# Performance work log

Hardware: AMD Instinct MI355X
Metric: run time of the kernel (lower is better)

The kernel has to match this reference:

```python
import jax, jax.numpy as jnp
import numpy as np

B, H, W, DIM, HEADS, WS = 32, 56, 56, 192, 6, 7
KD = DIM // HEADS          # key_dim = head_dim = 32 (attn_ratio=1.0 -> d = KD, dh = DIM)
DH = KD * HEADS
HQKV = DH + 2 * KD * HEADS # 576
L = H * W
HIDDEN = 4 * DIM
NWIN = (H // WS) * (W // WS)
NTOK = WS * WS
SCALE = KD ** -0.5


def _bias_idxs(ws):
    pts = [(i, j) for i in range(ws) for j in range(ws)]
    offs, idxs = {}, []
    for p1 in pts:
        for p2 in pts:
            o = (abs(p1[0] - p2[0]), abs(p1[1] - p2[1]))
            if o not in offs:
                offs[o] = len(offs)
            idxs.append(offs[o])
    return np.asarray(idxs, np.int32).reshape(ws * ws, ws * ws), len(offs)

BIAS_IDX, NOFF = _bias_idxs(WS)  # [49,49], 49 distinct offsets


def _ln(x, g, b, eps=1e-5):
    m = x.mean(-1, keepdims=True)
    v = jnp.mean((x - m) ** 2, -1, keepdims=True)
    return (x - m) * jax.lax.rsqrt(v + eps) * g + b


def setup_inputs() -> dict:
    key = jax.random.key(0)
    ks = jax.random.split(key, 8)
    f32 = jnp.float32
    return {
        "x": jax.random.normal(ks[0], (B, L, DIM), f32),
        "ln1_g": jnp.ones((DIM,), f32), "ln1_b": jnp.zeros((DIM,), f32),
        "qkv_w": jax.random.normal(ks[1], (DIM, HQKV), f32) * 0.02,
        "qkv_b": jnp.zeros((HQKV,), f32),
        "proj_w": jax.random.normal(ks[2], (DH, DIM), f32) * 0.02,
        "proj_b": jnp.zeros((DIM,), f32),
        "attn_bias": jax.random.normal(ks[3], (HEADS, NOFF), f32) * 0.02,
        "conv_w": jax.random.normal(ks[4], (DIM, 1, 3, 3), f32) * 0.1,  # depthwise OIHW
        "bn_g": jnp.ones((DIM,), f32), "bn_b": jnp.zeros((DIM,), f32),
        "bn_m": jnp.zeros((DIM,), f32), "bn_v": jnp.ones((DIM,), f32),
        "ln2_g": jnp.ones((DIM,), f32), "ln2_b": jnp.zeros((DIM,), f32),
        "fc1_w": jax.random.normal(ks[5], (DIM, HIDDEN), f32) * 0.02,
        "fc1_b": jnp.zeros((HIDDEN,), f32),
        "fc2_w": jax.random.normal(ks[6], (HIDDEN, DIM), f32) * 0.02,
        "fc2_b": jnp.zeros((DIM,), f32),
    }


def reference(x, ln1_g, ln1_b, qkv_w, qkv_b, proj_w, proj_b, attn_bias,
              conv_w, bn_g, bn_b, bn_m, bn_v, ln2_g, ln2_b,
              fc1_w, fc1_b, fc2_w, fc2_b):
    # ---- window partition: [B,L,C] -> [B*nWin, 49, C] (H,W divisible by WS, no pad)
    xw = x.reshape(B, H // WS, WS, W // WS, WS, DIM)
    xw = xw.transpose(0, 1, 3, 2, 4, 5).reshape(B * NWIN, NTOK, DIM)
    # ---- attention (pre-LN inside Attention module)
    h = _ln(xw, ln1_g, ln1_b)
    qkv = (h @ qkv_w + qkv_b).reshape(B * NWIN, NTOK, HEADS, 3 * KD)
    qkv = qkv.transpose(0, 2, 1, 3)                      # [Bw, heads, N, 3*KD]
    q, k, v = qkv[..., :KD], qkv[..., KD:2 * KD], qkv[..., 2 * KD:]
    bias = attn_bias[:, BIAS_IDX]                        # [heads, 49, 49] gathered table
    scores = jnp.einsum('bhnd,bhmd->bhnm', q, k) * SCALE + bias[None]
    a = jax.nn.softmax(scores, axis=-1)
    o = jnp.einsum('bhnm,bhmd->bhnd', a, v)
    o = o.transpose(0, 2, 1, 3).reshape(B * NWIN, NTOK, DH)
    o = o @ proj_w + proj_b
    # ---- window unpartition -> [B,L,C], residual add
    o = o.reshape(B, H // WS, W // WS, WS, WS, DIM)
    o = o.transpose(0, 1, 3, 2, 4, 5).reshape(B, L, DIM)
    x = x + o
    # ---- depthwise 3x3 conv + BN (eval-mode) in NCHW
    xc = x.transpose(0, 2, 1).reshape(B, DIM, H, W)
    xc = jax.lax.conv_general_dilated(
        xc, conv_w, window_strides=(1, 1), padding=[(1, 1), (1, 1)],
        feature_group_count=DIM, dimension_numbers=('NCHW', 'OIHW', 'NCHW'))
    inv = jax.lax.rsqrt(bn_v + 1e-5)
    xc = (xc - bn_m[None, :, None, None]) * (inv * bn_g)[None, :, None, None] + bn_b[None, :, None, None]
    x = xc.reshape(B, DIM, L).transpose(0, 2, 1)
    # ---- MLP (LN -> fc1 -> GELU(exact) -> fc2) with residual
    h2 = _ln(x, ln2_g, ln2_b)
    h2 = jax.nn.gelu(h2 @ fc1_w + fc1_b, approximate=False)
    h2 = h2 @ fc2_w + fc2_b
    return x + h2
```

## Files before the change

kernel.cpp:

```cpp
#include <hip/hip_runtime.h>
#include <hip/hip_bf16.h>

#define DIMC 192
#define LTOT 3136

using bf16x8 = __attribute__((ext_vector_type(8))) short;
using f32x4  = __attribute__((ext_vector_type(4))) float;

static __device__ __forceinline__ unsigned short f2bf(float f) {
  unsigned u = __builtin_bit_cast(unsigned, f);
  u = (u + 0x7FFFu + ((u >> 16) & 1u)) >> 16;
  return (unsigned short)u;
}
static __device__ __forceinline__ float bf2f(unsigned short u) {
  unsigned v = ((unsigned)u) << 16;
  return __builtin_bit_cast(float, v);
}
static __device__ __forceinline__ int iabs(int a) { return a < 0 ? -a : a; }

static __device__ __forceinline__ void gload16(const unsigned short* g, unsigned short* lds) {
  __builtin_amdgcn_global_load_lds(
      (const __attribute__((address_space(1))) void*)g,
      (__attribute__((address_space(3))) void*)lds, 16, 0, 0);
}

__global__ __launch_bounds__(256) void prep_k(
    const float* __restrict__ qkv_w, const float* __restrict__ proj_w,
    const float* __restrict__ fc1_w, const float* __restrict__ fc2_w,
    const float* __restrict__ conv_w,
    const float* __restrict__ bn_g, const float* __restrict__ bn_b,
    const float* __restrict__ bn_m, const float* __restrict__ bn_v,
    unsigned short* __restrict__ qkvT, unsigned short* __restrict__ projT,
    unsigned short* __restrict__ fc1T, unsigned short* __restrict__ fc2T,
    float* __restrict__ convT, float* __restrict__ bnsc, float* __restrict__ bnsh)
{
  int idx = blockIdx.x * 256 + threadIdx.x;
  if (idx < 122880) { int n = idx / 192, k = idx % 192;
    qkvT[idx] = (n < 576) ? f2bf(qkv_w[k * 576 + n]) : 0; return; }
  idx -= 122880;
  if (idx < 49152)  { int n = idx / 192, k = idx % 192;
    projT[idx] = (n < 192) ? f2bf(proj_w[k * 192 + n]) : 0; return; }
  idx -= 49152;
  if (idx < 147456) { int n = idx / 192, k = idx % 192;
    fc1T[idx] = f2bf(fc1_w[k * 768 + n]); return; }
  idx -= 147456;
  if (idx < 196608) { int n = idx / 768, k = idx % 768;
    fc2T[idx] = (n < 192) ? f2bf(fc2_w[k * 192 + n]) : 0; return; }
  idx -= 196608;
  if (idx < 1728)   { int tap = idx / 192, c = idx % 192; convT[idx] = conv_w[c * 9 + tap]; return; }
  idx -= 1728;
  if (idx < 192) {
    float s = bn_g[idx] * rsqrtf(bn_v[idx] + 1e-5f);
    bnsc[idx] = s; bnsh[idx] = bn_b[idx] - bn_m[idx] * s;
  }
}

__global__ __launch_bounds__(256) void ln1_k(
    const float* __restrict__ x, const float* __restrict__ g,
    const float* __restrict__ b, unsigned short* __restrict__ h1)
{
  const int grp = threadIdx.x >> 6, l = threadIdx.x & 63;
  const int m = blockIdx.x * 4 + grp;
  const int w = m / 49, t = m % 49;
  const int bb = w >> 6, win = w & 63;
  const int lpix = ((win >> 3) * 7 + t / 7) * 56 + (win & 7) * 7 + t % 7;
  const float* row = x + ((size_t)bb * LTOT + lpix) * DIMC;
  const bool act = l < 48;
  const int c = l * 4;
  float4 v = make_float4(0.f, 0.f, 0.f, 0.f);
  if (act) v = *(const float4*)(row + c);
  float s = v.x + v.y + v.z + v.w;
  float ss = v.x * v.x + v.y * v.y + v.z * v.z + v.w * v.w;
  #pragma unroll
  for (int off = 1; off < 64; off <<= 1) { s += __shfl_xor(s, off); ss += __shfl_xor(ss, off); }
  float mean = s * (1.f / 192.f);
  float rstd = rsqrtf(ss * (1.f / 192.f) - mean * mean + 1e-5f);
  if (act) {
    float4 gg = *(const float4*)(g + c);
    float4 bv = *(const float4*)(b + c);
    ushort4 o;
    o.x = f2bf((v.x - mean) * rstd * gg.x + bv.x);
    o.y = f2bf((v.y - mean) * rstd * gg.y + bv.y);
    o.z = f2bf((v.z - mean) * rstd * gg.z + bv.z);
    o.w = f2bf((v.w - mean) * rstd * gg.w + bv.w);
    *(ushort4*)(h1 + (size_t)m * DIMC + c) = o;
  }
}

__global__ __launch_bounds__(256) void qkvg_k(
    const unsigned short* __restrict__ h1, const unsigned short* __restrict__ qkvT,
    const float* __restrict__ qkv_b, unsigned short* __restrict__ qkv)
{
  __shared__ unsigned short Wc[12288];
  const int tid = threadIdx.x;
  const int l = tid & 63, wv = tid >> 6;
  const int u = l >> 4, ll = l & 15;
  const int m0 = blockIdx.x * 64;

  bf16x8 areg[6];
  {
    const unsigned short* arow = h1 + (size_t)(m0 + wv * 16 + ll) * 192;
    #pragma unroll
    for (int kk = 0; kk < 6; ++kk)
      areg[kk] = *(const bf16x8*)(arow + kk * 32 + u * 8);
  }
  for (int c = 0; c < 9; ++c) {
    if (c) __syncthreads();
    const char* Wg = (const char*)(qkvT + (size_t)c * 64 * 192);
    #pragma unroll
    for (int i = 0; i < 6; ++i) {
      int ob = i * 4096 + tid * 16;
      int r = ob / 384, cc = ob % 384;
      int cs = cc ^ ((r & 7) << 4);
      gload16((const unsigned short*)(Wg + r * 384 + cs), &Wc[ob >> 1]);
    }
    __syncthreads();
    f32x4 p1[4] = {};
    #pragma unroll
    for (int kk = 0; kk < 6; ++kk) {
      int cb = (kk * 64 + u * 16) ^ ((ll & 7) << 4);
      #pragma unroll
      for (int nf = 0; nf < 4; ++nf) {
        bf16x8 bfr = *(const bf16x8*)((const char*)Wc + (nf * 16 + ll) * 384 + cb);
        p1[nf] = __builtin_amdgcn_mfma_f32_16x16x32_bf16(areg[kk], bfr, p1[nf], 0, 0, 0);
      }
    }
    #pragma unroll
    for (int nf = 0; nf < 4; ++nf)
    #pragma unroll
    for (int r = 0; r < 4; ++r) {
      int m = m0 + wv * 16 + u * 4 + r;
      int n = c * 64 + nf * 16 + ll;
      qkv[(size_t)m * 576 + n] = f2bf(p1[nf][r] + qkv_b[n]);
    }
  }
}

__global__ __launch_bounds__(256) void attnp_k(
    const unsigned short* __restrict__ qkv, const float* __restrict__ attn_bias,
    const unsigned short* __restrict__ projT, const float* __restrict__ proj_b,
    const float* __restrict__ x, unsigned short* __restrict__ x1b)
{
  __shared__ unsigned short Qs[2560];
  __shared__ unsigned short Ks[2560];
  __shared__ unsigned short Vt[2304];
  __shared__ unsigned short Ps[4608];
  __shared__ float bias_s[52];
  const int tid = threadIdx.x;
  const int l = tid & 63, wv = tid >> 6;
  const int u = l >> 4, ll = l & 15;
  const int w = blockIdx.x, b = w >> 6, win = w & 63;
  const f32x4 fz = {0.f, 0.f, 0.f, 0.f};

  for (int i = tid; i < 15 * 40; i += 256) {
    Qs[(49 + i / 40) * 40 + i % 40] = 0;
    Ks[(49 + i / 40) * 40 + i % 40] = 0;
  }
  for (int i = tid; i < 32 * 15; i += 256) Vt[(i / 15) * 72 + 49 + i % 15] = 0;

  f32x4 pacc[4][3] = {};

  for (int h = 0; h < 6; ++h) {
    __syncthreads();
    if (tid < 49) bias_s[tid] = attn_bias[h * 49 + tid];
    #pragma unroll
    for (int it = 0; it < 3; ++it) {
      int idx = tid + it * 256;
      if (idx < 588) {
        int row = idx / 12, g = idx % 12;
        int4 v = *(const int4*)&qkv[((size_t)w * 49 + row) * 576 + h * 96 + g * 8];
        if (g < 4) *(int4*)&Qs[row * 40 + g * 8] = v;
        else if (g < 8) *(int4*)&Ks[row * 40 + (g - 4) * 8] = v;
        else {
          union { int4 v4; unsigned short us[8]; } uu; uu.v4 = v;
          int d0 = (g - 8) * 8;
          #pragma unroll
          for (int e = 0; e < 8; ++e) Vt[(d0 + e) * 72 + row] = uu.us[e];
        }
      }
    }
    __syncthreads();

    {
      const int qr = wv * 16 + ll;
      const int qi = qr > 48 ? 48 : qr;
      bf16x8 qf = *(const bf16x8*)&Qs[(wv * 16 + ll) * 40 + u * 8];
      f32x4 sc[4];
      #pragma unroll
      for (int kt = 0; kt < 4; ++kt) {
        bf16x8 kf = *(const bf16x8*)&Ks[(kt * 16 + ll) * 40 + u * 8];
        sc[kt] = __builtin_amdgcn_mfma_f32_16x16x32_bf16(kf, qf, fz, 0, 0, 0);
      }
      float sv[4][4];
      float mx = -1e30f;
      #pragma unroll
      for (int kt = 0; kt < 4; ++kt)
        #pragma unroll
        for (int r = 0; r < 4; ++r) {
          int kr = kt * 16 + u * 4 + r;
          float val = -1e30f;
          if (kr < 49)
            val = sc[kt][r] * 0.17677669529663689f +
                  bias_s[iabs(qi / 7 - kr / 7) * 7 + iabs(qi % 7 - kr % 7)];
          sv[kt][r] = val;
          mx = fmaxf(mx, val);
        }
      mx = fmaxf(mx, __shfl_xor(mx, 16));
      mx = fmaxf(mx, __shfl_xor(mx, 32));
      float sum = 0.f;
      #pragma unroll
      for (int kt = 0; kt < 4; ++kt)
        #pragma unroll
        for (int r = 0; r < 4; ++r) {
          float p = __expf(sv[kt][r] - mx);
          sv[kt][r] = p; sum += p;
        }
      sum += __shfl_xor(sum, 16);
      sum += __shfl_xor(sum, 32);
      float inv = 1.f / sum;
      #pragma unroll
      for (int kt = 0; kt < 4; ++kt)
        #pragma unroll
        for (int r = 0; r < 4; ++r)
          Ps[(wv * 16 + ll) * 72 + kt * 16 + u * 4 + r] = f2bf(sv[kt][r] * inv);
    }
    __syncthreads();

    {
      f32x4 oa[2] = {fz, fz};
      #pragma unroll
      for (int kk = 0; kk < 2; ++kk) {
        bf16x8 pf = *(const bf16x8*)&Ps[(wv * 16 + ll) * 72 + kk * 32 + u * 8];
        #pragma unroll
        for (int nt = 0; nt < 2; ++nt) {
          bf16x8 vf = *(const bf16x8*)&Vt[(nt * 16 + ll) * 72 + kk * 32 + u * 8];
          oa[nt] = __builtin_amdgcn_mfma_f32_16x16x32_bf16(pf, vf, oa[nt], 0, 0, 0);
        }
      }
      #pragma unroll
      for (int nt = 0; nt < 2; ++nt)
        #pragma unroll
        for (int r = 0; r < 4; ++r)
          Qs[(wv * 16 + u * 4 + r) * 40 + nt * 16 + ll] = f2bf(oa[nt][r]);
    }
    __syncthreads();

    {
      bf16x8 af[4], bfr[3];
      #pragma unroll
      for (int mt = 0; mt < 4; ++mt)
        af[mt] = *(const bf16x8*)&Qs[(mt * 16 + ll) * 40 + u * 8];
      #pragma unroll
      for (int nf = 0; nf < 3; ++nf)
        bfr[nf] = *(const bf16x8*)&projT[(size_t)(wv * 48 + nf * 16 + ll) * 192 + h * 32 + u * 8];
      #pragma unroll
      for (int mt = 0; mt < 4; ++mt)
        #pragma unroll
        for (int nf = 0; nf < 3; ++nf)
          pacc[mt][nf] = __builtin_amdgcn_mfma_f32_16x16x32_bf16(af[mt], bfr[nf], pacc[mt][nf], 0, 0, 0);
    }
  }

  #pragma unroll
  for (int mt = 0; mt < 4; ++mt)
  #pragma unroll
  for (int r = 0; r < 4; ++r) {
    int m = mt * 16 + u * 4 + r;
    if (m < 49) {
      int lpix = ((win >> 3) * 7 + m / 7) * 56 + (win & 7) * 7 + m % 7;
      size_t base = ((size_t)b * LTOT + lpix) * DIMC;
      #pragma unroll
      for (int nf = 0; nf < 3; ++nf) {
        int n = wv * 48 + nf * 16 + ll;
        float val = pacc[mt][nf][r] + proj_b[n] + x[base + n];
        x1b[base + n] = f2bf(val);
      }
    }
  }
}

__global__ __launch_bounds__(256) void fmlp_k(
    const unsigned short* __restrict__ h2, const unsigned short* __restrict__ fc1T,
    const float* __restrict__ fc1_b, const unsigned short* __restrict__ fc2T,
    const float* __restrict__ fc2_b, const unsigned short* __restrict__ x2,
    float* __restrict__ out)
{
  __shared__ unsigned short W1[6144];
  __shared__ unsigned short W2[6144];
  __shared__ unsigned short P[2048];
  const int tid = threadIdx.x;
  const int l = tid & 63, wv = tid >> 6;
  const int u = l >> 4, ll = l & 15;
  const int m0 = blockIdx.x * 64;
  f32x4 acc[12] = {};

  bf16x8 areg[6];
  {
    const unsigned short* arow = h2 + (size_t)(m0 + wv * 16 + ll) * 192;
    #pragma unroll
    for (int kk = 0; kk < 6; ++kk)
      areg[kk] = *(const bf16x8*)(arow + kk * 32 + u * 8);
  }

  for (int c = 0; c < 24; ++c) {
    if (c) __syncthreads();
    const char* W1g = (const char*)(fc1T + (size_t)c * 32 * 192);
    #pragma unroll
    for (int i = 0; i < 3; ++i) {
      int ob = i * 4096 + tid * 16;
      int r = ob / 384, cc = ob % 384;
      int cs = cc ^ ((r & 7) << 4);
      gload16((const unsigned short*)(W1g + r * 384 + cs), &W1[ob >> 1]);
    }
    #pragma unroll
    for (int i = 0; i < 3; ++i) {
      int unit = i * 256 + tid;
      int r = unit >> 2, q = unit & 3;
      int4 vv = *(const int4*)&fc2T[(size_t)r * 768 + c * 32 + q * 8];
      *(int4*)((char*)W2 + r * 64 + ((q * 16) ^ ((r & 3) << 4))) = vv;
    }
    __syncthreads();

    {
      f32x4 p1[2] = {};
      #pragma unroll
      for (int kk = 0; kk < 6; ++kk) {
        int cb = (kk * 64 + u * 16) ^ ((ll & 7) << 4);
        #pragma unroll
        for (int nf = 0; nf < 2; ++nf) {
          bf16x8 bfr = *(const bf16x8*)((const char*)W1 + (nf * 16 + ll) * 384 + cb);
          p1[nf] = __builtin_amdgcn_mfma_f32_16x16x32_bf16(areg[kk], bfr, p1[nf], 0, 0, 0);
        }
      }
      #pragma unroll
      for (int nf = 0; nf < 2; ++nf)
      #pragma unroll
      for (int r = 0; r < 4; ++r) {
        int mrow = wv * 16 + u * 4 + r;
        int n = nf * 16 + ll;
        float v = p1[nf][r] + fc1_b[c * 32 + n];
        float gl = v / (1.f + __expf(-1.5957691216057308f * (v + 0.044715f * v * v * v)));
        *(unsigned short*)((char*)P + mrow * 64 + ((n * 2) ^ ((mrow & 3) << 4))) = f2bf(gl);
      }
    }
    {
      bf16x8 af2 = *(const bf16x8*)((const char*)P + (wv * 16 + ll) * 64 +
                                    ((u * 16) ^ ((ll & 3) << 4)));
      #pragma unroll
      for (int nt = 0; nt < 12; ++nt) {
        bf16x8 bfr = *(const bf16x8*)((const char*)W2 + (nt * 16 + ll) * 64 +
                                      ((u * 16) ^ ((ll & 3) << 4)));
        acc[nt] = __builtin_amdgcn_mfma_f32_16x16x32_bf16(af2, bfr, acc[nt], 0, 0, 0);
      }
    }
  }
  #pragma unroll
  for (int nt = 0; nt < 12; ++nt)
  #pragma unroll
  for (int r = 0; r < 4; ++r) {
    int m = m0 + wv * 16 + u * 4 + r;
    int n = nt * 16 + ll;
    size_t o = (size_t)m * 192 + n;
    out[o] = acc[nt][r] + fc2_b[n] + bf2f(x2[o]);
  }
}

__global__ __launch_bounds__(256) void conv_k(
    const unsigned short* __restrict__ x1b, const float* __restrict__ wT,
    const float* __restrict__ bnsc, const float* __restrict__ bnsh,
    const float* __restrict__ g2, const float* __restrict__ b2,
    unsigned short* __restrict__ x2, unsigned short* __restrict__ h2)
{
  const int bid = blockIdx.x;
  const int swz = (bid & 7) * 3136 + (bid >> 3);
  const int grp = threadIdx.x >> 6, l = threadIdx.x & 63;
  const int gid = swz * 4 + grp;
  const int b = gid / LTOT, p = gid % LTOT;
  const int i = p / 56, j = p % 56;
  const bool act = l < 48;
  const int c = l * 4;
  float4 acc = make_float4(0.f, 0.f, 0.f, 0.f);
  if (act) {
    #pragma unroll
    for (int di = -1; di <= 1; ++di) {
      int ni = i + di;
      if (ni < 0 || ni >= 56) continue;
      #pragma unroll
      for (int dj = -1; dj <= 1; ++dj) {
        int nj = j + dj;
        if (nj < 0 || nj >= 56) continue;
        ushort4 sv = *(const ushort4*)&x1b[((size_t)b * LTOT + ni * 56 + nj) * DIMC + c];
        float4 wv = *(const float4*)&wT[((di + 1) * 3 + (dj + 1)) * DIMC + c];
        acc.x += bf2f(sv.x) * wv.x; acc.y += bf2f(sv.y) * wv.y;
        acc.z += bf2f(sv.z) * wv.z; acc.w += bf2f(sv.w) * wv.w;
      }
    }
    float4 s4 = *(const float4*)&bnsc[c];
    float4 h4 = *(const float4*)&bnsh[c];
    acc.x = acc.x * s4.x + h4.x; acc.y = acc.y * s4.y + h4.y;
    acc.z = acc.z * s4.z + h4.z; acc.w = acc.w * s4.w + h4.w;
    ushort4 xv;
    xv.x = f2bf(acc.x); xv.y = f2bf(acc.y); xv.z = f2bf(acc.z); xv.w = f2bf(acc.w);
    *(ushort4*)&x2[(size_t)gid * DIMC + c] = xv;
  }
  float s = act ? acc.x + acc.y + acc.z + acc.w : 0.f;
  float ss = act ? acc.x * acc.x + acc.y * acc.y + acc.z * acc.z + acc.w * acc.w : 0.f;
  #pragma unroll
  for (int off = 1; off < 64; off <<= 1) { s += __shfl_xor(s, off); ss += __shfl_xor(ss, off); }
  float mean = s * (1.f / 192.f);
  float rstd = rsqrtf(ss * (1.f / 192.f) - mean * mean + 1e-5f);
  if (act) {
    float4 gg = *(const float4*)&g2[c];
    float4 bb = *(const float4*)&b2[c];
    ushort4 ov;
    ov.x = f2bf((acc.x - mean) * rstd * gg.x + bb.x);
    ov.y = f2bf((acc.y - mean) * rstd * gg.y + bb.y);
    ov.z = f2bf((acc.z - mean) * rstd * gg.z + bb.z);
    ov.w = f2bf((acc.w - mean) * rstd * gg.w + bb.w);
    *(ushort4*)&h2[(size_t)gid * DIMC + c] = ov;
  }
}

extern "C" void kernel_launch(void* const* d_in, const int* in_sizes, int n_in,
                              void* d_out, int out_size, void* d_ws, size_t ws_size,
                              hipStream_t stream) {
  const float* x      = (const float*)d_in[0];
  const float* ln1_g  = (const float*)d_in[1];
  const float* ln1_b  = (const float*)d_in[2];
  const float* qkv_w  = (const float*)d_in[3];
  const float* qkv_b  = (const float*)d_in[4];
  const float* proj_w = (const float*)d_in[5];
  const float* proj_b = (const float*)d_in[6];
  const float* attn_b = (const float*)d_in[7];
  const float* conv_w = (const float*)d_in[8];
  const float* bn_g   = (const float*)d_in[9];
  const float* bn_b   = (const float*)d_in[10];
  const float* bn_m   = (const float*)d_in[11];
  const float* bn_v   = (const float*)d_in[12];
  const float* ln2_g  = (const float*)d_in[13];
  const float* ln2_b  = (const float*)d_in[14];
  const float* fc1_w  = (const float*)d_in[15];
  const float* fc1_b  = (const float*)d_in[16];
  const float* fc2_w  = (const float*)d_in[17];
  const float* fc2_b  = (const float*)d_in[18];
  float* out = (float*)d_out;

  const size_t AOFF = 1048576, BOFF = AOFF + 115605504;
  const size_t NEEDED = BOFF + 38535168;
  if (ws_size < NEEDED) return;

  char* ws = (char*)d_ws;
  unsigned short* qkvT  = (unsigned short*)(ws);
  unsigned short* projT = (unsigned short*)(ws + 245760);
  unsigned short* fc1T  = (unsigned short*)(ws + 344064);
  unsigned short* fc2T  = (unsigned short*)(ws + 638976);
  float*          convT = (float*)(ws + 1032192);
  float*          bnsc  = (float*)(ws + 1039104);
  float*          bnsh  = (float*)(ws + 1039872);

  unsigned short* qkv = (unsigned short*)(ws + AOFF);
  unsigned short* x2  = (unsigned short*)(ws + AOFF);
  unsigned short* h2  = (unsigned short*)(ws + AOFF + 38535168);
  unsigned short* h1  = (unsigned short*)(ws + BOFF);
  unsigned short* x1b = (unsigned short*)(ws + BOFF);

  prep_k<<<2024, 256, 0, stream>>>(qkv_w, proj_w, fc1_w, fc2_w, conv_w,
                                   bn_g, bn_b, bn_m, bn_v,
                                   qkvT, projT, fc1T, fc2T, convT, bnsc, bnsh);
  ln1_k<<<25088, 256, 0, stream>>>(x, ln1_g, ln1_b, h1);
  qkvg_k<<<1568, 256, 0, stream>>>(h1, qkvT, qkv_b, qkv);
  attnp_k<<<2048, 256, 0, stream>>>(qkv, attn_b, projT, proj_b, x, x1b);
  conv_k<<<25088, 256, 0, stream>>>(x1b, convT, bnsc, bnsh, ln2_g, ln2_b, x2, h2);
  fmlp_k<<<1568, 256, 0, stream>>>(h2, fc1T, fc1_b, fc2T, fc2_b, x2, out);
}
```

Measured before the change: 379.9 us.

## Double-buffer fc1/fc2 weight tiles in fused MLP kernel to overlap loads

The fused MLP kernel now keeps two LDS buffers each for the fc1 and fc2 weight chunks. While chunk c is being computed, it issues the global-to-LDS loads for fc1 chunk c+1 and register loads for fc2 chunk c+1, writing the fc2 data to LDS after compute. This cuts the per-iteration barrier from two to one and hides load latency behind MFMA work. The cost is roughly double the LDS footprint, which may reduce blocks per CU, plus extra register pressure from holding the prefetched fc2 data.

```diff
diff --git a/kernel.cpp b/kernel.cpp
--- a/kernel.cpp
+++ b/kernel.cpp
@@ -285,8 +285,8 @@
     const float* __restrict__ fc2_b, const unsigned short* __restrict__ x2,
     float* __restrict__ out)
 {
-  __shared__ unsigned short W1[6144];
-  __shared__ unsigned short W2[6144];
+  __shared__ unsigned short W1[2][6144];
+  __shared__ unsigned short W2[2][6144];
   __shared__ unsigned short P[2048];
   const int tid = threadIdx.x;
   const int l = tid & 63, wv = tid >> 6;
@@ -302,24 +302,47 @@
       areg[kk] = *(const bf16x8*)(arow + kk * 32 + u * 8);
   }
 
-  for (int c = 0; c < 24; ++c) {
-    if (c) __syncthreads();
-    const char* W1g = (const char*)(fc1T + (size_t)c * 32 * 192);
+  {
+    const char* W1g = (const char*)(fc1T);
     #pragma unroll
     for (int i = 0; i < 3; ++i) {
       int ob = i * 4096 + tid * 16;
       int r = ob / 384, cc = ob % 384;
       int cs = cc ^ ((r & 7) << 4);
-      gload16((const unsigned short*)(W1g + r * 384 + cs), &W1[ob >> 1]);
+      gload16((const unsigned short*)(W1g + r * 384 + cs), &W1[0][ob >> 1]);
     }
     #pragma unroll
     for (int i = 0; i < 3; ++i) {
       int unit = i * 256 + tid;
       int r = unit >> 2, q = unit & 3;
-      int4 vv = *(const int4*)&fc2T[(size_t)r * 768 + c * 32 + q * 8];
-      *(int4*)((char*)W2 + r * 64 + ((q * 16) ^ ((r & 3) << 4))) = vv;
-    }
-    __syncthreads();
+      int4 vv = *(const int4*)&fc2T[(size_t)r * 768 + q * 8];
+      *(int4*)((char*)W2[0] + r * 64 + ((q * 16) ^ ((r & 3) << 4))) = vv;
+    }
+  }
+  __syncthreads();
+
+  for (int c = 0; c < 24; ++c) {
+    const int cur = c & 1;
+    int4 w2r0, w2r1, w2r2;
+    if (c < 23) {
+      const char* W1g = (const char*)(fc1T + (size_t)(c + 1) * 32 * 192);
+      #pragma unroll
+      for (int i = 0; i < 3; ++i) {
+        int ob = i * 4096 + tid * 16;
+        int r = ob / 384, cc = ob % 384;
+        int cs = cc ^ ((r & 7) << 4);
+        gload16((const unsigned short*)(W1g + r * 384 + cs), &W1[cur ^ 1][ob >> 1]);
+      }
+      {
+        int unit = tid;
+        int r = unit >> 2, q = unit & 3;
+        w2r0 = *(const int4*)&fc2T[(size_t)r * 768 + (c + 1) * 32 + q * 8];
+        unit = 256 + tid; r = unit >> 2; q = unit & 3;
+        w2r1 = *(const int4*)&fc2T[(size_t)r * 768 + (c + 1) * 32 + q * 8];
+        unit = 512 + tid; r = unit >> 2; q = unit & 3;
+        w2r2 = *(const int4*)&fc2T[(size_t)r * 768 + (c + 1) * 32 + q * 8];
+      }
+    }
 
     {
       f32x4 p1[2] = {};
@@ -328,7 +351,7 @@
         int cb = (kk * 64 + u * 16) ^ ((ll & 7) << 4);
         #pragma unroll
         for (int nf = 0; nf < 2; ++nf) {
-          bf16x8 bfr = *(const bf16x8*)((const char*)W1 + (nf * 16 + ll) * 384 + cb);
+          bf16x8 bfr = *(const bf16x8*)((const char*)W1[cur] + (nf * 16 + ll) * 384 + cb);
           p1[nf] = __builtin_amdgcn_mfma_f32_16x16x32_bf16(areg[kk], bfr, p1[nf], 0, 0, 0);
         }
       }
@@ -348,11 +371,21 @@
                                     ((u * 16) ^ ((ll & 3) << 4)));
       #pragma unroll
       for (int nt = 0; nt < 12; ++nt) {
-        bf16x8 bfr = *(const bf16x8*)((const char*)W2 + (nt * 16 + ll) * 64 +
+        bf16x8 bfr = *(const bf16x8*)((const char*)W2[cur] + (nt * 16 + ll) * 64 +
                                       ((u * 16) ^ ((ll & 3) << 4)));
         acc[nt] = __builtin_amdgcn_mfma_f32_16x16x32_bf16(af2, bfr, acc[nt], 0, 0, 0);
       }
     }
+    if (c < 23) {
+      int unit = tid;
+      int r = unit >> 2, q = unit & 3;
+      *(int4*)((char*)W2[cur ^ 1] + r * 64 + ((q * 16) ^ ((r & 3) << 4))) = w2r0;
+      unit = 256 + tid; r = unit >> 2; q = unit & 3;
+      *(int4*)((char*)W2[cur ^ 1] + r * 64 + ((q * 16) ^ ((r & 3) << 4))) = w2r1;
+      unit = 512 + tid; r = unit >> 2; q = unit & 3;
+      *(int4*)((char*)W2[cur ^ 1] + r * 64 + ((q * 16) ^ ((r & 3) << 4))) = w2r2;
+    }
+    __syncthreads();
   }
   #pragma unroll
   for (int nt = 0; nt < 12; ++nt)
```

New measurement: 392.3 us. 1.03x slower.
